# Performance work log

Measured on AMD Instinct MI355X. Metric: run time of the kernel, lower is better.

## Reference

```python
import jax, jax.numpy as jnp
import numpy as np
from functools import partial

@jax.custom_vjp
def binarize(w):
    # BinaryConnectDeterministic forward: sign(w)
    return jnp.sign(w)

def _bin_fwd(w):
    return jnp.sign(w), w

def _bin_bwd(w, g):
    # straight-through estimator: pass grad where |w| <= 1
    return (g * (jnp.abs(w) <= 1.0).astype(g.dtype),)

binarize.defvjp(_bin_fwd, _bin_bwd)

STRIDE = (1, 1)
PADDING = ((1, 1), (1, 1))
DILATION = (1, 1)
GROUPS = 1

def setup_inputs() -> dict:
    key = jax.random.key(0)
    k1, k2, k3 = jax.random.split(key, 3)
    x = jax.random.normal(k1, (32, 256, 56, 56), dtype=jnp.float32)
    # uniform(-1, 1) init as in reset_parameters
    weight = jax.random.uniform(k2, (256, 256, 3, 3), dtype=jnp.float32, minval=-1.0, maxval=1.0)
    bias = jax.random.uniform(k3, (256,), dtype=jnp.float32, minval=-1.0, maxval=1.0)
    return {"x": x, "weight": weight, "bias": bias}

def reference(x, weight, bias):
    w_bin = binarize(weight)  # {-1, 0, +1} weights (sign)
    out = jax.lax.conv_general_dilated(
        x, w_bin,
        window_strides=STRIDE,
        padding=PADDING,
        rhs_dilation=DILATION,
        dimension_numbers=("NCHW", "OIHW", "NCHW"),
        feature_group_count=GROUPS,
    )
    return out + bias[None, :, None, None]
```

## Files before the change

kernel.cpp:

```cpp
#include <hip/hip_runtime.h>
#include <hip/hip_bf16.h>
#include <stdint.h>

#define N_IMG 32
#define C_IN  256
#define HW    56
#define PIX   3136
#define M_TOT 100352
#define C_OUT 256
#define K_TOT 2304
#define HP    58
#define WPAD  58
#define OUT_IMG_STRIDE 802816

#define BM 224
#define BN 128
#define SLAB_PIX 348
#define SLAB_SLOTS (SLAB_PIX * 4)

typedef __attribute__((ext_vector_type(8))) short bf16x8_t;
typedef __attribute__((ext_vector_type(4))) float f32x4_t;

__global__ void border_zero_kernel(__hip_bfloat16* __restrict__ xpad) {
    int t = blockIdx.x * 256 + threadIdx.x;
    if (t >= 32 * 228 * 32) return;
    int n = t / (228 * 32);
    int r = t - n * (228 * 32);
    int px = r >> 5, part = r & 31;
    int hp, wp;
    if (px < 58)       { hp = 0;  wp = px; }
    else if (px < 116) { hp = 57; wp = px - 116 + 58; }
    else { int k = px - 116; hp = 1 + (k >> 1); wp = (k & 1) ? 57 : 0; }
    long e = (((long)n * HP + hp) * WPAD + wp) * C_IN + part * 8;
    *(uint4*)(xpad + e) = make_uint4(0u, 0u, 0u, 0u);
}

__global__ void xform_kernel(const float* __restrict__ x, __hip_bfloat16* __restrict__ xpad) {
    __shared__ float tile[64][65];
    int b   = blockIdx.x;
    int n   = b / 196;
    int rem = b - n * 196;
    int ct  = rem / 49;
    int pt  = rem - ct * 49;
    int c0 = ct * 64, p0 = pt * 64;
    int t = threadIdx.x;

    const float* xs = x + (size_t)n * C_IN * PIX;
    int pc = t & 63, cr = t >> 6;
#pragma unroll
    for (int it = 0; it < 16; ++it) {
        int c = c0 + it * 4 + cr;
        tile[it * 4 + cr][pc] = xs[(size_t)c * PIX + p0 + pc];
    }
    __syncthreads();
    int cl = t & 63, pr = t >> 6;
#pragma unroll
    for (int it = 0; it < 16; ++it) {
        int p = p0 + it * 4 + pr;
        int h = p / HW, w = p - h * HW;
        float v = tile[cl][it * 4 + pr];
        xpad[(((size_t)n * HP + (h + 1)) * WPAD + (w + 1)) * C_IN + c0 + cl] = __float2bfloat16(v);
    }
}

__global__ void wxform_kernel(const float* __restrict__ w, __hip_bfloat16* __restrict__ wt) {
    int i = blockIdx.x * 256 + threadIdx.x;
    if (i >= C_OUT * K_TOT) return;
    int cout = i / K_TOT;
    int r    = i - cout * K_TOT;
    int tap  = r >> 8;
    int c    = r & 255;
    float v = w[cout * 2304 + c * 9 + tap];
    float s = (v > 0.f) ? 1.f : ((v < 0.f) ? -1.f : 0.f);
    wt[i] = __float2bfloat16(s);
}

__global__ void __launch_bounds__(256, 2)
gemm_kernel(const __hip_bfloat16* __restrict__ xpad,
            const __hip_bfloat16* __restrict__ wt,
            const float* __restrict__ bias,
            float* __restrict__ out) {
    __shared__ __hip_bfloat16 slab[SLAB_PIX * 32];

    int bx = blockIdx.x;
    int g = bx >> 4, xg = bx & 7, nt = (bx >> 3) & 1;
    int mt = g * 8 + xg;
    int nimg = mt / 14, ti = mt - nimg * 14;
    int r0 = ti * 4;
    int n0 = nt * BN;

    int tid = threadIdx.x, lane = tid & 63, wid = tid >> 6;
    int wm = wid >> 1, wn = wid & 1;
    int ar = lane & 15;
    int kq = lane >> 4;

    int p0[7];
#pragma unroll
    for (int i = 0; i < 7; ++i) {
        int m = wm * 112 + i * 16 + ar;
        int dr = m / 56, wcol = m - dr * 56;
        p0[i] = dr * 58 + wcol;
    }
    long wb[4];
#pragma unroll
    for (int j = 0; j < 4; ++j) {
        int n = n0 + wn * 64 + j * 16 + ar;
        wb[j] = (long)n * K_TOT + kq * 8;
    }

    const __hip_bfloat16* srcBase = xpad + ((long)(nimg * HP + r0) * WPAD) * C_IN;

    f32x4_t acc[7][4] = {};

    for (int ch = 0; ch < 8; ++ch) {
        if (ch) __syncthreads();
#pragma unroll
        for (int it = 0; it < 6; ++it) {
            int s = it * 256 + tid;
            if (s < SLAB_SLOTS) {
                int p = s >> 2, q = s & 3;
                uint4 v = *(const uint4*)(srcBase + (long)p * C_IN + ch * 32
                                          + ((q ^ ((p >> 1) & 3)) * 8));
                *(uint4*)((char*)slab + s * 16) = v;
            }
        }
        __syncthreads();

#pragma unroll
        for (int t = 0; t < 9; ++t) {
            const int kh = t / 3, kw = t - kh * 3;
            const int dpx = kh * 58 + kw;
            bf16x8_t b[4];
#pragma unroll
            for (int j = 0; j < 4; ++j)
                b[j] = *(const bf16x8_t*)&wt[wb[j] + t * 256 + ch * 32];
            bf16x8_t a[7];
#pragma unroll
            for (int i = 0; i < 7; ++i) {
                int p = p0[i] + dpx;
                int off = (p << 5) + ((kq ^ ((p >> 1) & 3)) << 3);
                a[i] = *(const bf16x8_t*)&slab[off];
            }
#pragma unroll
            for (int i = 0; i < 7; ++i)
#pragma unroll
                for (int j = 0; j < 4; ++j)
                    acc[i][j] = __builtin_amdgcn_mfma_f32_16x16x32_bf16(a[i], b[j], acc[i][j], 0, 0, 0);
        }
    }

    int cn = lane & 15;
    int rq = (lane >> 4) * 4;
    long outb = (long)nimg * OUT_IMG_STRIDE + r0 * 56;
#pragma unroll
    for (int i = 0; i < 7; ++i) {
        int mb = wm * 112 + i * 16 + rq;
#pragma unroll
        for (int j = 0; j < 4; ++j) {
            int cout = n0 + wn * 64 + j * 16 + cn;
            float bv = bias[cout];
            f32x4_t v = acc[i][j];
            v[0] += bv; v[1] += bv; v[2] += bv; v[3] += bv;
            *(f32x4_t*)&out[outb + (long)cout * PIX + mb] = v;
        }
    }
}

extern "C" void kernel_launch(void* const* d_in, const int* in_sizes, int n_in,
                              void* d_out, int out_size, void* d_ws, size_t ws_size,
                              hipStream_t stream) {
    const float* x    = (const float*)d_in[0];
    const float* wgt  = (const float*)d_in[1];
    const float* bias = (const float*)d_in[2];
    float* out = (float*)d_out;

    __hip_bfloat16* xpad = (__hip_bfloat16*)d_ws;
    __hip_bfloat16* wt   = (__hip_bfloat16*)((char*)d_ws + 55115776);

    border_zero_kernel<<<dim3((32 * 228 * 32 + 255) / 256), dim3(256), 0, stream>>>(xpad);

    xform_kernel<<<dim3(N_IMG * 4 * 49), dim3(256), 0, stream>>>(x, xpad);

    wxform_kernel<<<dim3((C_OUT * K_TOT + 255) / 256), dim3(256), 0, stream>>>(wgt, wt);

    gemm_kernel<<<dim3((M_TOT / BM) * (C_OUT / BN)), dim3(256), 0, stream>>>(xpad, wt, bias, out);
}
```

Before: 349.2 us.

## Retile conv GEMM to 64-pixel by 256-channel blocks with full output-channel coverage

The implicit-GEMM tile changes from 224 pixels x 128 output channels to 64 pixels x 256 channels. Each block now covers all output channels, so the input slab is loaded once per pixel tile instead of twice. The slab shrinks to 5 padded rows, and the global load addresses are computed once before the channel loop. The smaller accumulator allows three blocks per CU and gives 1568 blocks instead of 896, which should improve occupancy and load balance. The trade-off is more weight traffic per output pixel and fewer MFMAs per slab-load barrier, with a block-index swizzle spreading blocks across images.

```diff
diff --git a/kernel.cpp b/kernel.cpp
--- a/kernel.cpp
+++ b/kernel.cpp
@@ -13,9 +13,10 @@
 #define WPAD  58
 #define OUT_IMG_STRIDE 802816
 
-#define BM 224
-#define BN 128
-#define SLAB_PIX 348
+#define BM 64
+#define BN 256
+#define SLAB_ROWS 5
+#define SLAB_PIX  (SLAB_ROWS * 58)
 #define SLAB_SLOTS (SLAB_PIX * 4)
 
 typedef __attribute__((ext_vector_type(8))) short bf16x8_t;
@@ -75,7 +76,7 @@
     wt[i] = __float2bfloat16(s);
 }
 
-__global__ void __launch_bounds__(256, 2)
+__global__ void __launch_bounds__(256, 3)
 gemm_kernel(const __hip_bfloat16* __restrict__ xpad,
             const __hip_bfloat16* __restrict__ wt,
             const float* __restrict__ bias,
@@ -83,44 +84,46 @@
     __shared__ __hip_bfloat16 slab[SLAB_PIX * 32];
 
     int bx = blockIdx.x;
-    int g = bx >> 4, xg = bx & 7, nt = (bx >> 3) & 1;
-    int mt = g * 8 + xg;
-    int nimg = mt / 14, ti = mt - nimg * 14;
-    int r0 = ti * 4;
-    int n0 = nt * BN;
+    int b2 = (bx & 7) * 196 + (bx >> 3);
+    int n  = b2 / 49;
+    int pt = b2 - n * 49;
+    int rA = (8 * pt) / 7;
 
-    int tid = threadIdx.x, lane = tid & 63, wid = tid >> 6;
-    int wm = wid >> 1, wn = wid & 1;
+    int tid = threadIdx.x, lane = tid & 63, wn = tid >> 6;
     int ar = lane & 15;
     int kq = lane >> 4;
 
-    int p0[7];
+    int lp0[4];
 #pragma unroll
-    for (int i = 0; i < 7; ++i) {
-        int m = wm * 112 + i * 16 + ar;
-        int dr = m / 56, wcol = m - dr * 56;
-        p0[i] = dr * 58 + wcol;
+    for (int i = 0; i < 4; ++i) {
+        int px = pt * 64 + i * 16 + ar;
+        int r = px / 56, c = px - r * 56;
+        lp0[i] = (r - rA) * 58 + c;
     }
-    long wb[4];
+    int wb[4];
 #pragma unroll
-    for (int j = 0; j < 4; ++j) {
-        int n = n0 + wn * 64 + j * 16 + ar;
-        wb[j] = (long)n * K_TOT + kq * 8;
+    for (int j = 0; j < 4; ++j)
+        wb[j] = (wn * 64 + j * 16 + ar) * K_TOT + kq * 8;
+
+    int gi[5];
+#pragma unroll
+    for (int it = 0; it < 5; ++it) {
+        int s = it * 256 + tid;
+        int p = s >> 2, q = s & 3;
+        int dr = p / 58, wc = p - dr * 58;
+        int qs = q ^ ((p >> 1) & 3);
+        gi[it] = ((n * HP + rA + dr) * WPAD + wc) * C_IN + qs * 8;
     }
 
-    const __hip_bfloat16* srcBase = xpad + ((long)(nimg * HP + r0) * WPAD) * C_IN;
-
-    f32x4_t acc[7][4] = {};
+    f32x4_t acc[4][4] = {};
 
     for (int ch = 0; ch < 8; ++ch) {
         if (ch) __syncthreads();
 #pragma unroll
-        for (int it = 0; it < 6; ++it) {
+        for (int it = 0; it < 5; ++it) {
             int s = it * 256 + tid;
-            if (s < SLAB_SLOTS) {
-                int p = s >> 2, q = s & 3;
-                uint4 v = *(const uint4*)(srcBase + (long)p * C_IN + ch * 32
-                                          + ((q ^ ((p >> 1) & 3)) * 8));
+            if (it < 4 || s < SLAB_SLOTS) {
+                uint4 v = *(const uint4*)(xpad + (long)gi[it] + ch * 32);
                 *(uint4*)((char*)slab + s * 16) = v;
             }
         }
@@ -134,15 +137,15 @@
 #pragma unroll
             for (int j = 0; j < 4; ++j)
                 b[j] = *(const bf16x8_t*)&wt[wb[j] + t * 256 + ch * 32];
-            bf16x8_t a[7];
+            bf16x8_t a[4];
 #pragma unroll
-            for (int i = 0; i < 7; ++i) {
-                int p = p0[i] + dpx;
+            for (int i = 0; i < 4; ++i) {
+                int p = lp0[i] + dpx;
                 int off = (p << 5) + ((kq ^ ((p >> 1) & 3)) << 3);
                 a[i] = *(const bf16x8_t*)&slab[off];
             }
 #pragma unroll
-            for (int i = 0; i < 7; ++i)
+            for (int i = 0; i < 4; ++i)
 #pragma unroll
                 for (int j = 0; j < 4; ++j)
                     acc[i][j] = __builtin_amdgcn_mfma_f32_16x16x32_bf16(a[i], b[j], acc[i][j], 0, 0, 0);
@@ -151,13 +154,13 @@
 
     int cn = lane & 15;
     int rq = (lane >> 4) * 4;
-    long outb = (long)nimg * OUT_IMG_STRIDE + r0 * 56;
+    long outb = (long)n * OUT_IMG_STRIDE + pt * 64;
 #pragma unroll
-    for (int i = 0; i < 7; ++i) {
-        int mb = wm * 112 + i * 16 + rq;
+    for (int i = 0; i < 4; ++i) {
+        int mb = i * 16 + rq;
 #pragma unroll
         for (int j = 0; j < 4; ++j) {
-            int cout = n0 + wn * 64 + j * 16 + cn;
+            int cout = wn * 64 + j * 16 + cn;
             float bv = bias[cout];
             f32x4_t v = acc[i][j];
             v[0] += bv; v[1] += bv; v[2] += bv; v[3] += bv;
@@ -183,5 +186,5 @@
 
     wxform_kernel<<<dim3((C_OUT * K_TOT + 255) / 256), dim3(256), 0, stream>>>(wgt, wt);
 
-    gemm_kernel<<<dim3((M_TOT / BM) * (C_OUT / BN)), dim3(256), 0, stream>>>(xpad, wt, bias, out);
+    gemm_kernel<<<dim3(N_IMG * 49), dim3(256), 0, stream>>>(xpad, wt, bias, out);
 }
```

After: 437.1 us. +25.2%, slower.
